# Optimization experiments

Measured on AMD Instinct MI355X. Metric: run time of the kernel, lower is better.

## Reference

```python
import jax, jax.numpy as jnp
import numpy as np

B, N, D, H = 8, 1025, 768, 12
PRE = 1            # prefix (CLS) tokens
P = N - PRE        # patch tokens
HD = D // H
EPS = 1e-6


def setup_inputs() -> dict:
    key = jax.random.key(0)
    ks = jax.random.split(key, 8)
    x = jax.random.normal(ks[0], (B, N, D), dtype=jnp.float32)
    graph = jax.random.uniform(ks[1], (B, P, P), dtype=jnp.float32)
    transferability = jax.random.uniform(ks[2], (B, P), dtype=jnp.float32)
    Wqkv = jax.random.normal(ks[3], (3 * D, D), dtype=jnp.float32) * 0.02
    bqkv = jnp.zeros((3 * D,), dtype=jnp.float32)
    Wproj = jax.random.normal(ks[4], (D, D), dtype=jnp.float32) * 0.02
    bproj = jnp.zeros((D,), dtype=jnp.float32)
    return {"x": x, "graph": graph, "transferability": transferability,
            "Wqkv": Wqkv, "bqkv": bqkv, "Wproj": Wproj, "bproj": bproj,
            "prefix_tokens": PRE}


def _build_mask(graph, transferability, prefix_tokens, n_tokens):
    # patch_weights: [B, P]
    pw = transferability / (jnp.sum(transferability, axis=1, keepdims=True) + EPS)
    b, p = pw.shape
    pre = prefix_tokens
    # Block layout: [[1s (pre,pre), pw broadcast (pre,P)], [pw[:,None] (P,pre), graph]]
    top_left = jnp.ones((b, pre, pre), dtype=graph.dtype)
    top_right = jnp.broadcast_to(pw[:, None, :], (b, pre, p))
    bot_left = jnp.broadcast_to(pw[:, :, None], (b, p, pre))
    top = jnp.concatenate([top_left, top_right], axis=2)
    bot = jnp.concatenate([bot_left, graph], axis=2)
    return jnp.concatenate([top, bot], axis=1)  # [B, N, N]


def reference(x, graph, transferability, Wqkv, bqkv, Wproj, bproj, prefix_tokens):
    bsz, n, d = x.shape
    scale = HD ** -0.5
    qkv = x @ Wqkv.T + bqkv                          # [B, N, 3D]
    qkv = qkv.reshape(bsz, n, 3, H, HD).transpose(2, 0, 3, 1, 4)  # [3, B, H, N, hd]
    q, k, v = qkv[0], qkv[1], qkv[2]
    attn = jax.nn.softmax(jnp.einsum('bhid,bhjd->bhij', q, k) * scale, axis=-1)
    mask = _build_mask(graph, transferability, prefix_tokens, n)  # [B, N, N]
    attn = attn * mask[:, None, :, :]
    attn = attn / (jnp.sum(attn, axis=-1, keepdims=True) + EPS)
    out = jnp.einsum('bhij,bhjd->bhid', attn, v)     # [B, H, N, hd]
    out = out.transpose(0, 2, 1, 3).reshape(bsz, n, d)
    return out @ Wproj.T + bproj
```

## Files before the change

### kernel.cpp

```cpp
#include <hip/hip_runtime.h>
#include <stdint.h>

constexpr int Bq = 8, Nn = 1025, Dd = 768, Hh = 12, HDd = 64, Pp = 1024;
constexpr int NP = 1088;
constexpr int MROWS = Bq * Nn;
constexpr float EPSI = 1e-6f;

typedef __attribute__((ext_vector_type(8))) short bfrag;
typedef __attribute__((ext_vector_type(4))) float ffrag;
typedef __attribute__((ext_vector_type(4))) float f4;
typedef __attribute__((ext_vector_type(4))) unsigned short us4;

#define MFMA16(a, b, c) __builtin_amdgcn_mfma_f32_16x16x32_bf16((a), (b), (c), 0, 0, 0)

#if __has_builtin(__builtin_amdgcn_exp2f)
#define EXP2(x) __builtin_amdgcn_exp2f(x)
#else
#define EXP2(x) exp2f(x)
#endif

__device__ __forceinline__ unsigned short f2bf(float f) {
  union { float f; uint32_t u; } v{f};
  uint32_t u = v.u;
  return (unsigned short)((u + 0x7fffu + ((u >> 16) & 1u)) >> 16);
}
__device__ __forceinline__ float bf2f(unsigned short s) {
  union { uint32_t u; float f; } v; v.u = ((uint32_t)s) << 16; return v.f;
}
__device__ __forceinline__ uint32_t pkbf(float a, float b) {
  uint32_t r;
  asm("v_cvt_pk_bf16_f32 %0, %1, %2" : "=v"(r) : "v"(a), "v"(b));
  return r;
}

__device__ __forceinline__ void gload16(const void* g, void* l) {
  __builtin_amdgcn_global_load_lds((const __attribute__((address_space(1))) unsigned int*)g,
                                   (__attribute__((address_space(3))) unsigned int*)l, 16, 0, 0);
}

__global__ __launch_bounds__(256) void conv_kernel(const float* __restrict__ src,
                                                   unsigned short* __restrict__ dst, int n4) {
  int idx = blockIdx.x * blockDim.x + threadIdx.x;
  int stride = gridDim.x * blockDim.x;
  for (int i = idx; i < n4; i += stride) {
    f4 v = ((const f4*)src)[i];
    us4 o; o[0] = f2bf(v[0]); o[1] = f2bf(v[1]); o[2] = f2bf(v[2]); o[3] = f2bf(v[3]);
    ((us4*)dst)[i] = o;
  }
}

__global__ __launch_bounds__(256) void pw_kernel(const float* __restrict__ tr, float* __restrict__ pw) {
  int b = blockIdx.x;
  __shared__ float red[256];
  float s = 0.f;
  for (int j = threadIdx.x; j < Pp; j += 256) s += tr[b * Pp + j];
  red[threadIdx.x] = s; __syncthreads();
  for (int o = 128; o > 0; o >>= 1) { if (threadIdx.x < o) red[threadIdx.x] += red[threadIdx.x + o]; __syncthreads(); }
  float inv = 1.f / (red[0] + EPSI);
  for (int j = threadIdx.x; j < Pp; j += 256) pw[b * Pp + j] = tr[b * Pp + j] * inv;
}

__global__ __launch_bounds__(256) void mask_kernel(const float* __restrict__ graph,
                                                   const float* __restrict__ pw,
                                                   unsigned short* __restrict__ mask) {
  int i = blockIdx.x, b = blockIdx.y;
  unsigned short* mrow = mask + ((size_t)b * NP + i) * NP;
  if (i >= Nn) { for (int j = threadIdx.x; j < NP; j += 256) mrow[j] = 0; return; }
  if (i == 0) {
    for (int j = threadIdx.x; j < NP; j += 256) {
      float v = (j == 0) ? 1.f : (j <= Pp ? pw[b * Pp + j - 1] : 0.f);
      mrow[j] = f2bf(v);
    }
  } else {
    const float* grow = graph + ((size_t)b * Pp + (i - 1)) * Pp;
    for (int j = threadIdx.x; j < NP; j += 256) {
      float v = (j == 0) ? pw[b * Pp + i - 1] : (j <= Pp ? grow[j - 1] : 0.f);
      mrow[j] = f2bf(v);
    }
  }
}

__global__ __launch_bounds__(256) void padzero_kernel(unsigned short* __restrict__ Qo,
                                                      unsigned short* __restrict__ Ko,
                                                      unsigned short* __restrict__ Vo) {
  int bh = blockIdx.x;
  unsigned short* qp = Qo + ((size_t)bh * NP + Nn) * 64;
  unsigned short* kp = Ko + ((size_t)bh * NP + Nn) * 64;
  for (int idx = threadIdx.x; idx < (NP - Nn) * 64; idx += 256) { qp[idx] = 0; kp[idx] = 0; }
  unsigned short* vp = Vo + (size_t)bh * 64 * NP;
  for (int idx = threadIdx.x; idx < 64 * (NP - Nn); idx += 256) {
    int d = idx / (NP - Nn), j = Nn + (idx - d * (NP - Nn));
    vp[(size_t)d * NP + j] = 0;
  }
}

__device__ __forceinline__ void gemm_main(const unsigned short* __restrict__ A, int rowA0, int rowAmax,
                                          const unsigned short* __restrict__ Bw, int rowB0,
                                          uint4* lds, ffrag acc[4][4], int tid) {
  const int l = tid & 63, lm = l & 15, lg = l >> 4, w = tid >> 6, wr = w >> 1, wc = w & 1;
  const unsigned short* aS[4]; const unsigned short* bS[4];
#pragma unroll
  for (int q = 0; q < 4; q++) {
    int c = tid + 256 * q, r = c >> 3, p = c & 7, g = p ^ (r & 7);
    int ra = rowA0 + r; if (ra > rowAmax) ra = rowAmax;
    aS[q] = A + (size_t)ra * 768 + 8 * g;
    bS[q] = Bw + (size_t)(rowB0 + r) * 768 + 8 * g;
  }
  uint4* buf0 = lds;
  uint4* buf1 = lds + 2048;
#pragma unroll
  for (int q = 0; q < 4; q++) {
    gload16(aS[q], buf0 + tid + 256 * q);
    gload16(bS[q], buf0 + 1024 + tid + 256 * q);
    aS[q] += 64; bS[q] += 64;
  }
  asm volatile("s_waitcnt vmcnt(0)" ::: "memory");
  __builtin_amdgcn_sched_barrier(0);
  __builtin_amdgcn_s_barrier();
#pragma unroll 1
  for (int kt = 0; kt < 12; kt++) {
    uint4* cur = (kt & 1) ? buf1 : buf0;
    uint4* nxt = (kt & 1) ? buf0 : buf1;
    if (kt < 11) {
#pragma unroll
      for (int q = 0; q < 4; q++) {
        gload16(aS[q], nxt + tid + 256 * q);
        gload16(bS[q], nxt + 1024 + tid + 256 * q);
        aS[q] += 64; bS[q] += 64;
      }
    }
    const bfrag* LA = (const bfrag*)cur;
    const bfrag* LB = (const bfrag*)(cur + 1024);
    bfrag af[4][2], bf_[4][2];
#pragma unroll
    for (int am = 0; am < 4; am++) {
      int row = wr * 64 + am * 16 + lm;
      af[am][0] = LA[row * 8 + ((0 + lg) ^ (row & 7))];
      af[am][1] = LA[row * 8 + ((4 + lg) ^ (row & 7))];
    }
#pragma unroll
    for (int an = 0; an < 4; an++) {
      int row = wc * 64 + an * 16 + lm;
      bf_[an][0] = LB[row * 8 + ((0 + lg) ^ (row & 7))];
      bf_[an][1] = LB[row * 8 + ((4 + lg) ^ (row & 7))];
    }
#pragma unroll
    for (int am = 0; am < 4; am++)
#pragma unroll
      for (int an = 0; an < 4; an++) {
        acc[am][an] = MFMA16(af[am][0], bf_[an][0], acc[am][an]);
        acc[am][an] = MFMA16(af[am][1], bf_[an][1], acc[am][an]);
      }
    asm volatile("s_waitcnt vmcnt(0)" ::: "memory");
    __builtin_amdgcn_sched_barrier(0);
    __builtin_amdgcn_s_barrier();
  }
}

__device__ __forceinline__ int xcd_chunk_map(int orig, int nwg) {
  int qq = nwg >> 3, rr = nwg & 7;
  int xcd = orig & 7, idx = orig >> 3;
  int base = (xcd < rr) ? xcd * (qq + 1) : rr * (qq + 1) + (xcd - rr) * qq;
  return base + idx;
}

__global__ __launch_bounds__(256) void qkv_gemm_kernel(const unsigned short* __restrict__ X,
                                                       const unsigned short* __restrict__ W,
                                                       const float* __restrict__ bias,
                                                       unsigned short* __restrict__ Qo,
                                                       unsigned short* __restrict__ Ko,
                                                       unsigned short* __restrict__ Vo) {
  __shared__ uint4 lds[4096];
  int tid = threadIdx.x;
  int wg = xcd_chunk_map(blockIdx.x, 65 * 18);
  int xt = wg / 18, yt = wg - 18 * xt;
  ffrag zero4 = {0.f, 0.f, 0.f, 0.f};
  ffrag acc[4][4];
#pragma unroll
  for (int i = 0; i < 4; i++)
#pragma unroll
    for (int j = 0; j < 4; j++) acc[i][j] = zero4;
  gemm_main(X, xt * 128, MROWS - 1, W, yt * 128, lds, acc, tid);
  const int l = tid & 63, lm = l & 15, lg = l >> 4, w = tid >> 6, wr = w >> 1, wc = w & 1;
#pragma unroll
  for (int an = 0; an < 4; an++) {
    int gc = yt * 128 + wc * 64 + an * 16 + lm;
    int which = gc / 768, rr = gc - which * 768, h = rr >> 6, hd = rr & 63;
    float bv = bias[gc];
#pragma unroll
    for (int am = 0; am < 4; am++) {
      int grb = xt * 128 + wr * 64 + am * 16 + 4 * lg;
#pragma unroll
      for (int r = 0; r < 4; r++) {
        int gr = grb + r;
        if (gr >= MROWS) continue;
        int b = gr / Nn, i = gr - b * Nn;
        size_t bh = (size_t)(b * Hh + h);
        float v = acc[am][an][r] + bv;
        if (which == 0)      Qo[(bh * NP + i) * 64 + hd] = f2bf(v * 0.18033688f);
        else if (which == 1) Ko[(bh * NP + i) * 64 + hd] = f2bf(v);
        else                 Vo[(bh * 64 + hd) * NP + i] = f2bf(v);
      }
    }
  }
}

__global__ __launch_bounds__(256) void proj_gemm_kernel(const unsigned short* __restrict__ A,
                                                        const unsigned short* __restrict__ W,
                                                        const float* __restrict__ bias,
                                                        float* __restrict__ out) {
  __shared__ uint4 lds[4096];
  int tid = threadIdx.x;
  int wg = xcd_chunk_map(blockIdx.x, 65 * 6);
  int xt = wg / 6, yt = wg - 6 * xt;
  ffrag zero4 = {0.f, 0.f, 0.f, 0.f};
  ffrag acc[4][4];
#pragma unroll
  for (int i = 0; i < 4; i++)
#pragma unroll
    for (int j = 0; j < 4; j++) acc[i][j] = zero4;
  gemm_main(A, xt * 128, MROWS - 1, W, yt * 128, lds, acc, tid);
  const int l = tid & 63, lm = l & 15, lg = l >> 4, w = tid >> 6, wr = w >> 1, wc = w & 1;
#pragma unroll
  for (int an = 0; an < 4; an++) {
    int gc = yt * 128 + wc * 64 + an * 16 + lm;
    float bv = bias[gc];
#pragma unroll
    for (int am = 0; am < 4; am++) {
      int grb = xt * 128 + wr * 64 + am * 16 + 4 * lg;
#pragma unroll
      for (int r = 0; r < 4; r++) {
        int gr = grb + r;
        if (gr >= MROWS) continue;
        out[(size_t)gr * 768 + gc] = acc[am][an][r] + bv;
      }
    }
  }
}

__global__ __launch_bounds__(256) void attn_kernel(const unsigned short* __restrict__ Qg,
                                                   const unsigned short* __restrict__ Kg,
                                                   const unsigned short* __restrict__ Vg,
                                                   const unsigned short* __restrict__ Mg,
                                                   unsigned short* __restrict__ Og) {
  __shared__ uint4 smem[2560];
  int tid = threadIdx.x, w = tid >> 6, l = tid & 63, lm = l & 15, lg = l >> 4;
  int bx = blockIdx.x;
  int b = bx & 7, t5 = bx >> 3;
  int h = t5 % 12, ib = t5 / 12;
  size_t bh = (size_t)(b * Hh + h);
  const unsigned short* Qb = Qg + bh * NP * 64;
  const unsigned short* Kb = Kg + bh * NP * 64;
  const unsigned short* Vb = Vg + bh * 64 * NP;
  int i0 = ib * 64 + w * 16;
  int irow = i0 + lm;
  const unsigned short* Mrow = Mg + (size_t)b * NP * NP + (size_t)irow * NP;

  bfrag qf0 = *(const bfrag*)(Qb + (size_t)irow * 64 + 8 * lg);
  bfrag qf1 = *(const bfrag*)(Qb + (size_t)irow * 64 + 32 + 8 * lg);

  ffrag zero4 = {0.f, 0.f, 0.f, 0.f};
  ffrag oacc[4] = {zero4, zero4, zero4, zero4};
  float Tp = 0.f;

  int rS = tid >> 3, pS = tid & 7;
  int rS2 = rS + 32;
  const unsigned short* kS0 = Kb + (size_t)rS * 64 + 8 * (pS ^ (rS & 7));
  const unsigned short* kS1 = Kb + (size_t)rS2 * 64 + 8 * (pS ^ (rS2 & 7));
  const unsigned short* vS0 = Vb + (size_t)rS * NP + 8 * (pS ^ (rS & 7));
  const unsigned short* vS1 = Vb + (size_t)rS2 * NP + 8 * (pS ^ (rS2 & 7));

  char* Pbase = (char*)(smem + 2048) + w * 2048;

  gload16(kS0, smem + tid);
  gload16(kS1, smem + tid + 256);
  gload16(vS0, smem + 1024 + tid);
  gload16(vS1, smem + 1024 + tid + 256);
  us4 mva[4], mvb[4];
#pragma unroll
  for (int jm = 0; jm < 4; jm++) mva[jm] = *(const us4*)(Mrow + 16 * jm + 4 * lg);
  asm volatile("s_waitcnt vmcnt(0)" ::: "memory");
  __builtin_amdgcn_sched_barrier(0);
  __builtin_amdgcn_s_barrier();

#pragma unroll 1
  for (int t = 0; t < 17; t++) {
    int cb = (t & 1) << 9;
    if (t < 16) {
      int nb = ((t + 1) & 1) << 9;
      size_t ko = (size_t)(t + 1) * 4096;
      int vo = (t + 1) * 64;
      gload16(kS0 + ko, smem + nb + tid);
      gload16(kS1 + ko, smem + nb + tid + 256);
      gload16(vS0 + vo, smem + 1024 + nb + tid);
      gload16(vS1 + vo, smem + 1024 + nb + tid + 256);
#pragma unroll
      for (int jm = 0; jm < 4; jm++) mvb[jm] = *(const us4*)(Mrow + (t + 1) * 64 + 16 * jm + 4 * lg);
    }
    const bfrag* LK = (const bfrag*)(smem + cb);
    const bfrag* LV = (const bfrag*)(smem + 1024 + cb);

    ffrag s[4];
    __builtin_amdgcn_s_setprio(1);
#pragma unroll
    for (int jm = 0; jm < 4; jm++) {
      int row = jm * 16 + lm;
      bfrag a0 = LK[row * 8 + ((0 + lg) ^ (row & 7))];
      bfrag a1 = LK[row * 8 + ((4 + lg) ^ (row & 7))];
      ffrag a = zero4;
      a = MFMA16(a0, qf0, a);
      a = MFMA16(a1, qf1, a);
      s[jm] = a;
    }
    __builtin_amdgcn_s_setprio(0);
#pragma unroll
    for (int jm = 0; jm < 4; jm++) {
      float p0 = EXP2(s[jm][0]), p1 = EXP2(s[jm][1]), p2 = EXP2(s[jm][2]), p3 = EXP2(s[jm][3]);
      float q0 = p0 * bf2f(mva[jm][0]), q1 = p1 * bf2f(mva[jm][1]);
      float q2 = p2 * bf2f(mva[jm][2]), q3 = p3 * bf2f(mva[jm][3]);
      Tp += (q0 + q1) + (q2 + q3);
      uint2 pk; pk.x = pkbf(q0, q1); pk.y = pkbf(q2, q3);
      int cpos = (((jm << 1) | (lg >> 1)) ^ (lm & 7));
      *(uint2*)(Pbase + lm * 128 + cpos * 16 + 8 * (lg & 1)) = pk;
    }
    __builtin_amdgcn_s_setprio(1);
#pragma unroll
    for (int ks = 0; ks < 2; ks++) {
      bfrag pa = *(const bfrag*)(Pbase + lm * 128 + ((((ks << 2) | lg)) ^ (lm & 7)) * 16);
#pragma unroll
      for (int dm = 0; dm < 4; dm++) {
        int vrow = dm * 16 + lm;
        bfrag vb = LV[vrow * 8 + ((ks * 4 + lg) ^ (vrow & 7))];
        oacc[dm] = MFMA16(pa, vb, oacc[dm]);
      }
    }
    __builtin_amdgcn_s_setprio(0);
#pragma unroll
    for (int jm = 0; jm < 4; jm++) mva[jm] = mvb[jm];
    asm volatile("s_waitcnt vmcnt(0)" ::: "memory");
    __builtin_amdgcn_sched_barrier(0);
    __builtin_amdgcn_s_barrier();
  }
  Tp += __shfl_xor(Tp, 16); Tp += __shfl_xor(Tp, 32);
  float dn_row = 1.f / Tp;
  float dn[4];
#pragma unroll
  for (int r = 0; r < 4; r++) dn[r] = __shfl(dn_row, 4 * lg + r);
#pragma unroll
  for (int dm = 0; dm < 4; dm++)
#pragma unroll
    for (int r = 0; r < 4; r++) {
      int i = i0 + 4 * lg + r;
      if (i < Nn) Og[((size_t)(b * Nn + i)) * Dd + h * 64 + dm * 16 + lm] = f2bf(oacc[dm][r] * dn[r]);
    }
}

extern "C" void kernel_launch(void* const* d_in, const int* in_sizes, int n_in,
                              void* d_out, int out_size, void* d_ws, size_t ws_size,
                              hipStream_t stream) {
  const float* x      = (const float*)d_in[0];
  const float* graph  = (const float*)d_in[1];
  const float* transf = (const float*)d_in[2];
  const float* Wqkv   = (const float*)d_in[3];
  const float* bqkv   = (const float*)d_in[4];
  const float* Wproj  = (const float*)d_in[5];
  const float* bproj  = (const float*)d_in[6];
  float* out = (float*)d_out;
  char* ws = (char*)d_ws;

  unsigned short* xbf  = (unsigned short*)(ws + 0);
  unsigned short* wqb  = (unsigned short*)(ws + 12595200);
  unsigned short* wpb  = (unsigned short*)(ws + 16134144);
  unsigned short* Qb   = (unsigned short*)(ws + 17313792);
  unsigned short* Kb   = (unsigned short*)(ws + 30683136);
  unsigned short* Vb   = (unsigned short*)(ws + 44052480);
  float*          pw   = (float*)(ws + 57421824);
  unsigned short* mask = (unsigned short*)(ws + 57454592);
  unsigned short* aob  = xbf;

  conv_kernel<<<2048, 256, 0, stream>>>(x, xbf, (MROWS * Dd) / 4);
  conv_kernel<<<1728, 256, 0, stream>>>(Wqkv, wqb, (3 * Dd * Dd) / 4);
  conv_kernel<<<576, 256, 0, stream>>>(Wproj, wpb, (Dd * Dd) / 4);
  pw_kernel<<<Bq, 256, 0, stream>>>(transf, pw);
  mask_kernel<<<dim3(NP, Bq), 256, 0, stream>>>(graph, pw, mask);
  padzero_kernel<<<96, 256, 0, stream>>>(Qb, Kb, Vb);
  qkv_gemm_kernel<<<65 * 18, 256, 0, stream>>>(xbf, wqb, bqkv, Qb, Kb, Vb);
  attn_kernel<<<1632, 256, 0, stream>>>(Qb, Kb, Vb, mask, aob);
  proj_gemm_kernel<<<65 * 6, 256, 0, stream>>>(aob, wpb, bproj, out);
}
```

Before: 205.3 us.

## Triple-buffer K/V tiles in attention kernel with two-ahead prefetch

Converts the double-buffered K/V LDS staging into a three-stage ring that prefetches two tiles ahead and waits with a partial vmcnt instead of draining all loads each iteration. The mask values are now loaded at the top of each iteration rather than prefetched one step ahead. The aim is to hide more global-load latency behind MFMA work. In exchange, LDS per block grows, which may lower occupancy, and the mask load latency is now exposed within the same iteration.

```diff
diff --git a/kernel.cpp b/kernel.cpp
--- a/kernel.cpp
+++ b/kernel.cpp
@@ -243,7 +243,7 @@
                                                    const unsigned short* __restrict__ Vg,
                                                    const unsigned short* __restrict__ Mg,
                                                    unsigned short* __restrict__ Og) {
-  __shared__ uint4 smem[2560];
+  __shared__ uint4 smem[3584];
   int tid = threadIdx.x, w = tid >> 6, l = tid & 63, lm = l & 15, lg = l >> 4;
   int bx = blockIdx.x;
   int b = bx & 7, t5 = bx >> 3;
@@ -270,35 +270,42 @@
   const unsigned short* vS0 = Vb + (size_t)rS * NP + 8 * (pS ^ (rS & 7));
   const unsigned short* vS1 = Vb + (size_t)rS2 * NP + 8 * (pS ^ (rS2 & 7));
 
-  char* Pbase = (char*)(smem + 2048) + w * 2048;
-
-  gload16(kS0, smem + tid);
-  gload16(kS1, smem + tid + 256);
-  gload16(vS0, smem + 1024 + tid);
-  gload16(vS1, smem + 1024 + tid + 256);
-  us4 mva[4], mvb[4];
-#pragma unroll
-  for (int jm = 0; jm < 4; jm++) mva[jm] = *(const us4*)(Mrow + 16 * jm + 4 * lg);
-  asm volatile("s_waitcnt vmcnt(0)" ::: "memory");
+  char* Pbase = (char*)(smem + 3072) + w * 2048;
+
+  {
+    uint4* bp = smem;
+    gload16(kS0, bp + tid);        gload16(kS1, bp + tid + 256);
+    gload16(vS0, bp + 512 + tid);  gload16(vS1, bp + 512 + tid + 256);
+  }
+  __builtin_amdgcn_sched_barrier(0);
+  {
+    uint4* bp = smem + 1024;
+    gload16(kS0 + 4096, bp + tid);       gload16(kS1 + 4096, bp + tid + 256);
+    gload16(vS0 + 64, bp + 512 + tid);   gload16(vS1 + 64, bp + 512 + tid + 256);
+  }
+  __builtin_amdgcn_sched_barrier(0);
+  asm volatile("s_waitcnt vmcnt(8)" ::: "memory");
   __builtin_amdgcn_sched_barrier(0);
   __builtin_amdgcn_s_barrier();
 
+  int pc = 0;
 #pragma unroll 1
   for (int t = 0; t < 17; t++) {
-    int cb = (t & 1) << 9;
-    if (t < 16) {
-      int nb = ((t + 1) & 1) << 9;
-      size_t ko = (size_t)(t + 1) * 4096;
-      int vo = (t + 1) * 64;
-      gload16(kS0 + ko, smem + nb + tid);
-      gload16(kS1 + ko, smem + nb + tid + 256);
-      gload16(vS0 + vo, smem + 1024 + nb + tid);
-      gload16(vS1 + vo, smem + 1024 + nb + tid + 256);
-#pragma unroll
-      for (int jm = 0; jm < 4; jm++) mvb[jm] = *(const us4*)(Mrow + (t + 1) * 64 + 16 * jm + 4 * lg);
-    }
-    const bfrag* LK = (const bfrag*)(smem + cb);
-    const bfrag* LV = (const bfrag*)(smem + 1024 + cb);
+    us4 mva[4];
+#pragma unroll
+    for (int jm = 0; jm < 4; jm++) mva[jm] = *(const us4*)(Mrow + t * 64 + 16 * jm + 4 * lg);
+    __builtin_amdgcn_sched_barrier(0);
+    if (t < 15) {
+      int pf = pc + 2; if (pf > 2) pf -= 3;
+      uint4* bp = smem + pf * 1024;
+      size_t ko = (size_t)(t + 2) * 4096;
+      int vo = (t + 2) * 64;
+      gload16(kS0 + ko, bp + tid);       gload16(kS1 + ko, bp + tid + 256);
+      gload16(vS0 + vo, bp + 512 + tid); gload16(vS1 + vo, bp + 512 + tid + 256);
+    }
+    __builtin_amdgcn_sched_barrier(0);
+    const bfrag* LK = (const bfrag*)(smem + pc * 1024);
+    const bfrag* LV = (const bfrag*)(smem + pc * 1024 + 512);
 
     ffrag s[4];
     __builtin_amdgcn_s_setprio(1);
@@ -335,11 +342,14 @@
       }
     }
     __builtin_amdgcn_s_setprio(0);
-#pragma unroll
-    for (int jm = 0; jm < 4; jm++) mva[jm] = mvb[jm];
-    asm volatile("s_waitcnt vmcnt(0)" ::: "memory");
+    if (t < 15) {
+      asm volatile("s_waitcnt vmcnt(8)" ::: "memory");
+    } else {
+      asm volatile("s_waitcnt vmcnt(0)" ::: "memory");
+    }
     __builtin_amdgcn_sched_barrier(0);
     __builtin_amdgcn_s_barrier();
+    pc = (pc == 2) ? 0 : pc + 1;
   }
   Tp += __shfl_xor(Tp, 16); Tp += __shfl_xor(Tp, 32);
   float dn_row = 1.f / Tp;
```

After: 228.0 us. 11.0% more time.

## Process two 64-row query tiles per attention block to reuse K/V tiles

Applied to the files above, without the earlier changes.

Each attention workgroup now handles 128 query rows (two 64-row groups per wave) instead of 64, so every K/V tile staged in shared memory and the V fragments held in registers serve twice as many rows. The grid drops from 1632 to 864 blocks, and rows past the padded length are clamped. The mask prefetch one step ahead is replaced by loads issued within the current iteration, which may expose memory latency. The extra accumulators raise register pressure and lower block count, which could hurt occupancy and load balance.

```diff
diff --git a/kernel.cpp b/kernel.cpp
--- a/kernel.cpp
+++ b/kernel.cpp
@@ -252,16 +252,22 @@
   const unsigned short* Qb = Qg + bh * NP * 64;
   const unsigned short* Kb = Kg + bh * NP * 64;
   const unsigned short* Vb = Vg + bh * 64 * NP;
-  int i0 = ib * 64 + w * 16;
-  int irow = i0 + lm;
-  const unsigned short* Mrow = Mg + (size_t)b * NP * NP + (size_t)irow * NP;
-
-  bfrag qf0 = *(const bfrag*)(Qb + (size_t)irow * 64 + 8 * lg);
-  bfrag qf1 = *(const bfrag*)(Qb + (size_t)irow * 64 + 32 + 8 * lg);
+  int i0a = ib * 128 + w * 16;
+  int i0b = i0a + 64;
+  int irowa = i0a + lm; if (irowa > NP - 1) irowa = NP - 1;
+  int irowb = i0b + lm; if (irowb > NP - 1) irowb = NP - 1;
+  const unsigned short* Mrowa = Mg + (size_t)b * NP * NP + (size_t)irowa * NP;
+  const unsigned short* Mrowb = Mg + (size_t)b * NP * NP + (size_t)irowb * NP;
+
+  bfrag qa0 = *(const bfrag*)(Qb + (size_t)irowa * 64 + 8 * lg);
+  bfrag qa1 = *(const bfrag*)(Qb + (size_t)irowa * 64 + 32 + 8 * lg);
+  bfrag qb0 = *(const bfrag*)(Qb + (size_t)irowb * 64 + 8 * lg);
+  bfrag qb1 = *(const bfrag*)(Qb + (size_t)irowb * 64 + 32 + 8 * lg);
 
   ffrag zero4 = {0.f, 0.f, 0.f, 0.f};
-  ffrag oacc[4] = {zero4, zero4, zero4, zero4};
-  float Tp = 0.f;
+  ffrag oaccA[4] = {zero4, zero4, zero4, zero4};
+  ffrag oaccB[4] = {zero4, zero4, zero4, zero4};
+  float TpA = 0.f, TpB = 0.f;
 
   int rS = tid >> 3, pS = tid & 7;
   int rS2 = rS + 32;
@@ -274,51 +280,71 @@
 
   gload16(kS0, smem + tid);
   gload16(kS1, smem + tid + 256);
-  gload16(vS0, smem + 1024 + tid);
-  gload16(vS1, smem + 1024 + tid + 256);
-  us4 mva[4], mvb[4];
-#pragma unroll
-  for (int jm = 0; jm < 4; jm++) mva[jm] = *(const us4*)(Mrow + 16 * jm + 4 * lg);
+  gload16(vS0, smem + 512 + tid);
+  gload16(vS1, smem + 512 + tid + 256);
   asm volatile("s_waitcnt vmcnt(0)" ::: "memory");
   __builtin_amdgcn_sched_barrier(0);
   __builtin_amdgcn_s_barrier();
 
 #pragma unroll 1
   for (int t = 0; t < 17; t++) {
-    int cb = (t & 1) << 9;
+    int cb = (t & 1) << 10;
     if (t < 16) {
-      int nb = ((t + 1) & 1) << 9;
+      int nb = ((t + 1) & 1) << 10;
       size_t ko = (size_t)(t + 1) * 4096;
       int vo = (t + 1) * 64;
       gload16(kS0 + ko, smem + nb + tid);
       gload16(kS1 + ko, smem + nb + tid + 256);
-      gload16(vS0 + vo, smem + 1024 + nb + tid);
-      gload16(vS1 + vo, smem + 1024 + nb + tid + 256);
-#pragma unroll
-      for (int jm = 0; jm < 4; jm++) mvb[jm] = *(const us4*)(Mrow + (t + 1) * 64 + 16 * jm + 4 * lg);
+      gload16(vS0 + vo, smem + nb + 512 + tid);
+      gload16(vS1 + vo, smem + nb + 512 + tid + 256);
+    }
+    int j0 = t * 64;
+    us4 mvA[4], mvB[4];
+#pragma unroll
+    for (int jm = 0; jm < 4; jm++) {
+      mvA[jm] = *(const us4*)(Mrowa + j0 + 16 * jm + 4 * lg);
+      mvB[jm] = *(const us4*)(Mrowb + j0 + 16 * jm + 4 * lg);
     }
     const bfrag* LK = (const bfrag*)(smem + cb);
-    const bfrag* LV = (const bfrag*)(smem + 1024 + cb);
-
-    ffrag s[4];
-    __builtin_amdgcn_s_setprio(1);
+    const bfrag* LV = (const bfrag*)(smem + cb + 512);
+
+    bfrag ka[4], kb2[4];
 #pragma unroll
     for (int jm = 0; jm < 4; jm++) {
       int row = jm * 16 + lm;
-      bfrag a0 = LK[row * 8 + ((0 + lg) ^ (row & 7))];
-      bfrag a1 = LK[row * 8 + ((4 + lg) ^ (row & 7))];
+      ka[jm]  = LK[row * 8 + ((0 + lg) ^ (row & 7))];
+      kb2[jm] = LK[row * 8 + ((4 + lg) ^ (row & 7))];
+    }
+    ffrag sa[4], sb[4];
+    __builtin_amdgcn_s_setprio(1);
+#pragma unroll
+    for (int jm = 0; jm < 4; jm++) {
       ffrag a = zero4;
-      a = MFMA16(a0, qf0, a);
-      a = MFMA16(a1, qf1, a);
-      s[jm] = a;
+      a = MFMA16(ka[jm], qa0, a);
+      a = MFMA16(kb2[jm], qa1, a);
+      sa[jm] = a;
+      ffrag bb = zero4;
+      bb = MFMA16(ka[jm], qb0, bb);
+      bb = MFMA16(kb2[jm], qb1, bb);
+      sb[jm] = bb;
     }
     __builtin_amdgcn_s_setprio(0);
+
+    bfrag vf[2][4];
+#pragma unroll
+    for (int ks = 0; ks < 2; ks++)
+#pragma unroll
+      for (int dm = 0; dm < 4; dm++) {
+        int vrow = dm * 16 + lm;
+        vf[ks][dm] = LV[vrow * 8 + ((ks * 4 + lg) ^ (vrow & 7))];
+      }
+
 #pragma unroll
     for (int jm = 0; jm < 4; jm++) {
-      float p0 = EXP2(s[jm][0]), p1 = EXP2(s[jm][1]), p2 = EXP2(s[jm][2]), p3 = EXP2(s[jm][3]);
-      float q0 = p0 * bf2f(mva[jm][0]), q1 = p1 * bf2f(mva[jm][1]);
-      float q2 = p2 * bf2f(mva[jm][2]), q3 = p3 * bf2f(mva[jm][3]);
-      Tp += (q0 + q1) + (q2 + q3);
+      float p0 = EXP2(sa[jm][0]), p1 = EXP2(sa[jm][1]), p2 = EXP2(sa[jm][2]), p3 = EXP2(sa[jm][3]);
+      float q0 = p0 * bf2f(mvA[jm][0]), q1 = p1 * bf2f(mvA[jm][1]);
+      float q2 = p2 * bf2f(mvA[jm][2]), q3 = p3 * bf2f(mvA[jm][3]);
+      TpA += (q0 + q1) + (q2 + q3);
       uint2 pk; pk.x = pkbf(q0, q1); pk.y = pkbf(q2, q3);
       int cpos = (((jm << 1) | (lg >> 1)) ^ (lm & 7));
       *(uint2*)(Pbase + lm * 128 + cpos * 16 + 8 * (lg & 1)) = pk;
@@ -328,30 +354,48 @@
     for (int ks = 0; ks < 2; ks++) {
       bfrag pa = *(const bfrag*)(Pbase + lm * 128 + ((((ks << 2) | lg)) ^ (lm & 7)) * 16);
 #pragma unroll
-      for (int dm = 0; dm < 4; dm++) {
-        int vrow = dm * 16 + lm;
-        bfrag vb = LV[vrow * 8 + ((ks * 4 + lg) ^ (vrow & 7))];
-        oacc[dm] = MFMA16(pa, vb, oacc[dm]);
-      }
+      for (int dm = 0; dm < 4; dm++) oaccA[dm] = MFMA16(pa, vf[ks][dm], oaccA[dm]);
     }
     __builtin_amdgcn_s_setprio(0);
-#pragma unroll
-    for (int jm = 0; jm < 4; jm++) mva[jm] = mvb[jm];
+
+#pragma unroll
+    for (int jm = 0; jm < 4; jm++) {
+      float p0 = EXP2(sb[jm][0]), p1 = EXP2(sb[jm][1]), p2 = EXP2(sb[jm][2]), p3 = EXP2(sb[jm][3]);
+      float q0 = p0 * bf2f(mvB[jm][0]), q1 = p1 * bf2f(mvB[jm][1]);
+      float q2 = p2 * bf2f(mvB[jm][2]), q3 = p3 * bf2f(mvB[jm][3]);
+      TpB += (q0 + q1) + (q2 + q3);
+      uint2 pk; pk.x = pkbf(q0, q1); pk.y = pkbf(q2, q3);
+      int cpos = (((jm << 1) | (lg >> 1)) ^ (lm & 7));
+      *(uint2*)(Pbase + lm * 128 + cpos * 16 + 8 * (lg & 1)) = pk;
+    }
+    __builtin_amdgcn_s_setprio(1);
+#pragma unroll
+    for (int ks = 0; ks < 2; ks++) {
+      bfrag pa = *(const bfrag*)(Pbase + lm * 128 + ((((ks << 2) | lg)) ^ (lm & 7)) * 16);
+#pragma unroll
+      for (int dm = 0; dm < 4; dm++) oaccB[dm] = MFMA16(pa, vf[ks][dm], oaccB[dm]);
+    }
+    __builtin_amdgcn_s_setprio(0);
+
     asm volatile("s_waitcnt vmcnt(0)" ::: "memory");
     __builtin_amdgcn_sched_barrier(0);
     __builtin_amdgcn_s_barrier();
   }
-  Tp += __shfl_xor(Tp, 16); Tp += __shfl_xor(Tp, 32);
-  float dn_row = 1.f / Tp;
-  float dn[4];
-#pragma unroll
-  for (int r = 0; r < 4; r++) dn[r] = __shfl(dn_row, 4 * lg + r);
+  TpA += __shfl_xor(TpA, 16); TpA += __shfl_xor(TpA, 32);
+  TpB += __shfl_xor(TpB, 16); TpB += __shfl_xor(TpB, 32);
+  float dnA_row = 1.f / TpA;
+  float dnB_row = 1.f / TpB;
+  float dnA[4], dnB[4];
+#pragma unroll
+  for (int r = 0; r < 4; r++) { dnA[r] = __shfl(dnA_row, 4 * lg + r); dnB[r] = __shfl(dnB_row, 4 * lg + r); }
 #pragma unroll
   for (int dm = 0; dm < 4; dm++)
 #pragma unroll
     for (int r = 0; r < 4; r++) {
-      int i = i0 + 4 * lg + r;
-      if (i < Nn) Og[((size_t)(b * Nn + i)) * Dd + h * 64 + dm * 16 + lm] = f2bf(oacc[dm][r] * dn[r]);
+      int ia = i0a + 4 * lg + r;
+      if (ia < Nn) Og[((size_t)(b * Nn + ia)) * Dd + h * 64 + dm * 16 + lm] = f2bf(oaccA[dm][r] * dnA[r]);
+      int ibr = i0b + 4 * lg + r;
+      if (ibr < Nn) Og[((size_t)(b * Nn + ibr)) * Dd + h * 64 + dm * 16 + lm] = f2bf(oaccB[dm][r] * dnB[r]);
     }
 }
 
@@ -385,6 +429,6 @@
   mask_kernel<<<dim3(NP, Bq), 256, 0, stream>>>(graph, pw, mask);
   padzero_kernel<<<96, 256, 0, stream>>>(Qb, Kb, Vb);
   qkv_gemm_kernel<<<65 * 18, 256, 0, stream>>>(xbf, wqb, bqkv, Qb, Kb, Vb);
-  attn_kernel<<<1632, 256, 0, stream>>>(Qb, Kb, Vb, mask, aob);
+  attn_kernel<<<864, 256, 0, stream>>>(Qb, Kb, Vb, mask, aob);
   proj_gemm_kernel<<<65 * 6, 256, 0, stream>>>(aob, wpb, bproj, out);
 }
```

After: 209.5 us. +2.0%, slower.
